# Optimization experiments

Hardware: AMD Instinct MI355X
Metric: run time of the kernel (lower is better)

Reference implementation:

```python
import jax, jax.numpy as jnp
import numpy as np

SQRT_HALF = 0.7071067811865476
DILATIONS = [3 ** (i % 4) for i in range(8)]  # [1,3,9,27,1,3,9,27]


def conv1d(x, w, b, dilation=1):
    # x: [B, Cin, L], w: [Cout, Cin, K], 'same' padding
    out = jax.lax.conv_general_dilated(
        x, w, window_strides=(1,), padding='SAME',
        rhs_dilation=(dilation,),
        dimension_numbers=('NCH', 'OIH', 'NCH'))
    return out + b[None, :, None]


def encoder(x, enc_start_w, enc_start_b, glu_w, glu_b, enc_end_w, enc_end_b):
    # EncoderAny (eval mode -> dropout is identity)
    h = conv1d(x, enc_start_w, enc_start_b)                  # [B, mid, N]
    for i in range(len(DILATIONS)):
        g = conv1d(h, glu_w[i], glu_b[i], dilation=DILATIONS[i])  # [B, 2*mid, N]
        a, b = jnp.split(g, 2, axis=1)
        h = (h + a * jax.nn.sigmoid(b)) * SQRT_HALF           # GLU + residual
    out = conv1d(h, enc_end_w, enc_end_b)                     # [B, 2*d, N]
    K, V = jnp.split(out, 2, axis=1)                          # each [B, d, N]
    return K, V


def reference(in_s, in_t, c_t,
              enc_start_w, enc_start_b, glu_w, glu_b, enc_end_w, enc_end_b,
              wc_pre, w_pre, b_pre, wc_post, w_post, b_post):
    # ---- encoder: source -> K, V ----
    K_s, V_s = encoder(in_s, enc_start_w, enc_start_b, glu_w, glu_b,
                       enc_end_w, enc_end_b)                  # [B, d, N] each
    d = K_s.shape[1]

    # ---- pre-decoder: target + speaker code -> Q ----
    h_t = in_t + jnp.einsum('bc,cd->bd', c_t, wc_pre)[:, :, None]  # [B, D, T]
    Q_t = conv1d(h_t, w_pre, b_pre)                           # [B, d, T]

    # ---- custom attention: softmax over SOURCE axis (dim=1) ----
    scores = jnp.einsum('bdn,bdt->bnt', K_s, Q_t) / jnp.sqrt(
        jnp.asarray(d, dtype=K_s.dtype))                      # [B, N, T]
    A = jax.nn.softmax(scores, axis=1)                        # softmax over N
    R = jnp.einsum('bdn,bnt->bdt', V_s, A)                    # [B, d, T]

    # concat with Q (dropout p=0.9 in training; eval/deterministic -> identity)
    R = jnp.concatenate([R, Q_t], axis=1)                     # [B, 2d, T]

    # ---- post-decoder: attended features + speaker code -> y ----
    h_r = R + jnp.einsum('bc,cd->bd', c_t, wc_post)[:, :, None]
    y = conv1d(h_r, w_post, b_post)                           # [B, D, T]
    return y, A


def setup_inputs() -> dict:
    key = jax.random.key(0)
    ks = jax.random.split(key, 16)
    B, D, N, T = 16, 240, 2048, 2048
    mid, d, C = 512, 512, 8
    L = len(DILATIONS)

    def w(k, shape, fan_in):
        return (jax.random.normal(k, shape, dtype=jnp.float32)
                / jnp.sqrt(jnp.asarray(fan_in, jnp.float32)))

    return {
        'in_s': jax.random.normal(ks[0], (B, D, N), dtype=jnp.float32),
        'in_t': jax.random.normal(ks[1], (B, D, T), dtype=jnp.float32),
        'c_t': jax.random.normal(ks[2], (B, C), dtype=jnp.float32),
        'enc_start_w': w(ks[3], (mid, D, 1), D),
        'enc_start_b': jnp.zeros((mid,), jnp.float32),
        'glu_w': w(ks[4], (L, 2 * mid, mid, 5), mid * 5),
        'glu_b': jnp.zeros((L, 2 * mid), jnp.float32),
        'enc_end_w': w(ks[5], (2 * d, mid, 1), mid),
        'enc_end_b': jnp.zeros((2 * d,), jnp.float32),
        'wc_pre': w(ks[6], (C, D), C),
        'w_pre': w(ks[7], (d, D, 1), D),
        'b_pre': jnp.zeros((d,), jnp.float32),
        'wc_post': w(ks[8], (C, 2 * d), C),
        'w_post': w(ks[9], (D, 2 * d, 1), 2 * d),
        'b_post': jnp.zeros((D,), jnp.float32),
    }
```

## Files before the change

### kernel.cpp

```cpp
#include <hip/hip_runtime.h>
#include <cstdint>
#include <cstddef>

typedef unsigned short u16;
typedef __attribute__((ext_vector_type(8))) short short8;
typedef __attribute__((ext_vector_type(4))) float f32x4;

static constexpr int BB = 16, DIN = 240, NN = 2048, TT = 2048;
static constexpr long long Y_SIZE = (long long)BB * DIN * TT;
static constexpr float SQRT_HALF_F = 0.70710678118654752440f;
static constexpr int HPAD = 64;
static constexpr int HROWS = NN + 2 * HPAD;

#define DEVI __device__ __forceinline__

DEVI u16 f2bf(float f) {
    unsigned u = __builtin_bit_cast(unsigned, f);
    u += 0x7FFFu + ((u >> 16) & 1u);
    return (u16)(u >> 16);
}
DEVI float bf2f(u16 h) {
    unsigned u = ((unsigned)h) << 16;
    return __builtin_bit_cast(float, u);
}

DEVI void gld16(const void* g, const void* l) {
    __builtin_amdgcn_global_load_lds(
        (const __attribute__((address_space(1))) unsigned int*)g,
        (__attribute__((address_space(3))) unsigned int*)l, 16, 0, 0);
}

DEVI int glu_perm(int g) {
    int tile = g >> 8, r = g & 255;
    int wcq = r >> 6, r2 = r & 63;
    int n = r2 >> 4, fr = r2 & 15;
    return tile * 128 + wcq * 32 + (n >> 1) * 16 + fr + (n & 1) * 512;
}

struct GemmP {
    const u16* A; long long a_bstride; int lda;
    const u16* Bw; long long b_bstride; long long b_tapstride; int ldb;
    int ntaps; int shift0; int dshift; int Kt; int ks_log2;
    void* out; long long o_bstride; int ldc;
    const float* bias; int bias_bstride;
    float scale;
    int store_ncols;
};

#define FENCE() asm volatile("" ::: "memory")
#define SBAR()  do { FENCE(); __builtin_amdgcn_s_barrier(); FENCE(); } while (0)

template <int OUTK>
__global__ __launch_bounds__(512, 2)
void gemm256(GemmP p, int tilesM, int tilesN) {
    __shared__ __align__(16) u16 As[2][256 * 64];
    __shared__ __align__(16) u16 Bs[2][256 * 64];
    const int tid = threadIdx.x;
    const int lane = tid & 63;
    const int wv = tid >> 6;
    const int wr = wv >> 2, wcq = wv & 3;
    const int fr = lane & 15, fq = lane >> 4;

    const int nwg = gridDim.x;
    int widx = (blockIdx.x & 7) * (nwg >> 3) + (blockIdx.x >> 3);
    const int mt = widx % tilesM; widx /= tilesM;
    const int nt = widx % tilesN;
    const int bz = widx / tilesN;
    const int n0 = mt * 256, c0 = nt * 256;

    const int lda = p.lda, ldb = p.ldb;
    const u16* Abase = p.A + (long long)bz * p.a_bstride;
    const u16* Bbase = p.Bw + (long long)bz * p.b_bstride;
    const int kmask = (1 << p.ks_log2) - 1;
    const int tot = p.ntaps << p.ks_log2;

    f32x4 acc[8][4];
#pragma unroll
    for (int m = 0; m < 8; ++m)
#pragma unroll
        for (int n = 0; n < 4; ++n) acc[m][n] = (f32x4){0.f, 0.f, 0.f, 0.f};

    const int srow = lane >> 3, sslot = lane & 7;
    const int js = (sslot ^ srow) << 3;
    const int sr0 = wv * 16 + srow;

    const long long sA8 = 8LL * lda, sAh = 128LL * lda;
    const long long sB8 = 8LL * ldb, sBh = 128LL * ldb;
    const long long dAtap = (long long)p.dshift * lda - (long long)kmask * 64;
    const long long dBtap = p.b_tapstride - (long long)kmask * 64;

    auto aAddr = [&](int t) -> const u16* {
        int tap = t >> p.ks_log2;
        return Abase + (long long)(n0 + p.shift0 + tap * p.dshift + sr0) * lda
               + ((t & kmask) << 6) + js;
    };
    auto bAddr = [&](int t) -> const u16* {
        int tap = t >> p.ks_log2;
        return Bbase + (long long)tap * p.b_tapstride
               + (long long)(c0 + sr0) * ldb + ((t & kmask) << 6) + js;
    };

    u16* uA = &As[0][wv * 1024];
    u16* uB = &Bs[0][wv * 1024];

    {
        const u16* a0 = aAddr(0);
        gld16(a0, uA);              gld16(a0 + sA8, uA + 512);
        gld16(a0 + sAh, uA + 8192); gld16(a0 + sAh + sA8, uA + 8192 + 512);
        const u16* b0 = bAddr(0);
        gld16(b0, uB);              gld16(b0 + sB8, uB + 512);
        gld16(b0 + sBh, uB + 8192); gld16(b0 + sBh + sB8, uB + 8192 + 512);
        const u16* b1 = bAddr(1);
        gld16(b1, uB + 16384);              gld16(b1 + sB8, uB + 16384 + 512);
        gld16(b1 + sBh, uB + 16384 + 8192); gld16(b1 + sBh + sB8, uB + 16384 + 8192 + 512);
    }
    const u16* aP = aAddr(1);
    const u16* bP = bAddr(2);
    asm volatile("s_waitcnt vmcnt(4)" ::: "memory");
    __builtin_amdgcn_s_barrier();
    FENCE();

    const int aoff0 = (wr * 128 + fr) * 64 + ((fq ^ (fr & 7)) << 3);
    const int aoff1 = (wr * 128 + fr) * 64 + (((4 + fq) ^ (fr & 7)) << 3);
    const int boff0 = (wcq * 64 + fr) * 64 + ((fq ^ (fr & 7)) << 3);
    const int boff1 = (wcq * 64 + fr) * 64 + (((4 + fq) ^ (fr & 7)) << 3);

    short8 af0[4][2], af1[4][2], bf0[2][2], bf1[2][2];

#define READ_AQ(DEST, MQ)                                                      \
    _Pragma("unroll")                                                          \
    for (int mi = 0; mi < 4; ++mi) {                                           \
        DEST[mi][0] = *(const short8*)&Ab[aoff0 + ((MQ) * 64 + mi * 16) * 64]; \
        DEST[mi][1] = *(const short8*)&Ab[aoff1 + ((MQ) * 64 + mi * 16) * 64]; \
    }
#define READ_BQ(BF, NQ)                                                        \
    _Pragma("unroll")                                                          \
    for (int ni = 0; ni < 2; ++ni) {                                           \
        BF[ni][0] = *(const short8*)&Bb[boff0 + ((NQ) * 32 + ni * 16) * 64];   \
        BF[ni][1] = *(const short8*)&Bb[boff1 + ((NQ) * 32 + ni * 16) * 64];   \
    }
#define MFMA_Q2(MQ, NQ, AF, BF)                                                \
    __builtin_amdgcn_s_setprio(1);                                             \
    _Pragma("unroll")                                                          \
    for (int mi = 0; mi < 4; ++mi) {                                           \
        _Pragma("unroll")                                                      \
        for (int ni = 0; ni < 2; ++ni) {                                       \
            _Pragma("unroll")                                                  \
            for (int kk = 0; kk < 2; ++kk)                                     \
                acc[(MQ) * 4 + mi][(NQ) * 2 + ni] =                            \
                    __builtin_amdgcn_mfma_f32_16x16x32_bf16(                   \
                        AF[mi][kk], BF[ni][kk],                                \
                        acc[(MQ) * 4 + mi][(NQ) * 2 + ni], 0, 0, 0);           \
        }                                                                      \
    }                                                                          \
    __builtin_amdgcn_s_setprio(0)

#define TILEBODY(BUF_, DO_A_, DO_B_, STEPA_, STEPB_, VM_)                      \
  {                                                                            \
    const u16* Ab = &As[BUF_][0];                                              \
    const u16* Bb = &Bs[BUF_][0];                                              \
    \
    READ_AQ(af0, 0);                                                           \
    READ_BQ(bf0, 0);                                                           \
    READ_BQ(bf1, 1);                                                           \
    if (DO_A_) { gld16(aP, uA + ((BUF_) ^ 1) * 16384);                         \
                 gld16(aP + sA8, uA + ((BUF_) ^ 1) * 16384 + 512); }           \
    MFMA_Q2(0, 0, af0, bf0);                                                   \
    if (DO_A_) { gld16(aP + sAh, uA + ((BUF_) ^ 1) * 16384 + 8192);            \
                 gld16(aP + sAh + sA8, uA + ((BUF_) ^ 1) * 16384 + 8192 + 512);\
                 aP += (STEPA_); }                                             \
    MFMA_Q2(0, 1, af0, bf1);                                                   \
    SBAR();                                                                    \
                  \
    READ_AQ(af1, 1);                                                           \
    if (DO_B_) { gld16(bP, uB + (BUF_) * 16384);                               \
                 gld16(bP + sB8, uB + (BUF_) * 16384 + 512); }                 \
    MFMA_Q2(1, 1, af1, bf1);                                                   \
    if (DO_B_) { gld16(bP + sBh, uB + (BUF_) * 16384 + 8192);                  \
                 gld16(bP + sBh + sB8, uB + (BUF_) * 16384 + 8192 + 512);      \
                 bP += (STEPB_); }                                             \
    MFMA_Q2(1, 0, af1, bf0);                                                   \
    if ((VM_) == 4) asm volatile("s_waitcnt vmcnt(4)" ::: "memory");           \
    else if ((VM_) == 0) asm volatile("s_waitcnt vmcnt(0)" ::: "memory");      \
    SBAR();                                                                    \
  }

    int t = 0;
    for (; t + 3 < tot; t += 2) {
        const long long stA1 = (((t + 2) & kmask) != 0) ? 64 : dAtap;
        const long long stA2 = (((t + 3) & kmask) != 0) ? 64 : dAtap;
        const long long stB1 = (((t + 3) & kmask) != 0) ? 64 : dBtap;
        const long long stB2 = (((t + 4) & kmask) != 0) ? 64 : dBtap;
        TILEBODY(0, 1, 1, stA1, stB1, 4);
        TILEBODY(1, 1, 1, stA2, stB2, 4);
    }
    TILEBODY(0, 1, 0, 0, 0, 0);
    TILEBODY(1, 0, 0, 0, 0, -1);
#undef READ_AQ
#undef READ_BQ
#undef MFMA_Q2
#undef TILEBODY

    if constexpr (OUTK == 4) {
        const float* bp = p.bias;
#pragma unroll
        for (int m = 0; m < 8; ++m) {
#pragma unroll
            for (int pr = 0; pr < 2; ++pr) {
                int ca = c0 + wcq * 64 + (2 * pr) * 16 + fr;
                int chan = (c0 >> 1) + wcq * 32 + pr * 16 + fr;
                float biasa = bp[ca], biasb = bp[ca + 16];
#pragma unroll
                for (int r = 0; r < 4; ++r) {
                    int row = n0 + wr * 128 + m * 16 + fq * 4 + r;
                    float a = acc[m][2 * pr][r] + biasa;
                    float bq = acc[m][2 * pr + 1][r] + biasb;
                    float sig = 1.f / (1.f + __expf(-bq));
                    float h = bf2f(Abase[(long long)row * lda + chan]);
                    ((u16*)p.out)[(long long)bz * p.o_bstride + (long long)row * p.ldc + chan]
                        = f2bf((h + a * sig) * SQRT_HALF_F);
                }
            }
        }
        return;
    } else if constexpr (OUTK == 2) {
        const float* bias = p.bias + (long long)bz * p.bias_bstride;
#pragma unroll
        for (int m = 0; m < 8; ++m) {
#pragma unroll
            for (int n = 0; n < 4; ++n) {
                int col = c0 + wcq * 64 + n * 16 + fr;
                if (col >= p.store_ncols) continue;
                float cb = bias[col];
#pragma unroll
                for (int r = 0; r < 4; ++r) {
                    int row = n0 + wr * 128 + m * 16 + fq * 4 + r;
                    ((float*)p.out)[(long long)bz * p.o_bstride + (long long)col * p.ldc + row]
                        = acc[m][n][r] * p.scale + cb;
                }
            }
        }
        return;
    } else {
        const float* bias = p.bias ? p.bias + (long long)bz * p.bias_bstride : nullptr;
#pragma unroll
        for (int m = 0; m < 8; ++m) {
#pragma unroll
            for (int n = 0; n < 4; ++n) {
                int col = c0 + wcq * 64 + n * 16 + fr;
                float cb = (OUTK == 1 && bias) ? bias[col] : 0.f;
#pragma unroll
                for (int r = 0; r < 4; ++r) {
                    int row = n0 + wr * 128 + m * 16 + fq * 4 + r;
                    float v = acc[m][n][r] * p.scale + cb;
                    if (OUTK == 5) v += bias[row];
                    ((u16*)p.out)[(long long)bz * p.o_bstride + (long long)row * p.ldc + col]
                        = f2bf(v);
                }
            }
        }
    }
}


__global__ void cvt_glu(const float* src, u16* dst) {
    long long t = (long long)blockIdx.x * blockDim.x + threadIdx.x;
    const long long total = 8LL * 5 * 1024 * 512;
    if (t >= total) return;
    int i = (int)(t % 512); long long r = t / 512;
    int g = (int)(r % 1024); r /= 1024;
    int k = (int)(r % 5); int l = (int)(r / 5);
    int o = glu_perm(g);
    dst[t] = f2bf(src[(((long long)l * 1024 + o) * 512 + i) * 5 + k]);
}

__global__ void perm_bias(const float* gb, float* biasP) {
    int t = blockIdx.x * 256 + threadIdx.x;
    if (t >= 8 * 1024) return;
    int g = t & 1023, l = t >> 10;
    biasP[t] = gb[l * 1024 + glu_perm(g)];
}

__global__ void cvt_pad(const float* src, u16* dst, int Os, int Is, int Od, int Id) {
    long long t = (long long)blockIdx.x * blockDim.x + threadIdx.x;
    if (t >= (long long)Od * Id) return;
    int i = (int)(t % Id); int o = (int)(t / Id);
    float v = (o < Os && i < Is) ? src[(long long)o * Is + i] : 0.f;
    dst[t] = f2bf(v);
}

__global__ void transpose_in(const float* src, u16* dst, int Csrc, int Cdst, int Len) {
    __shared__ float tile[32][33];
    int b = blockIdx.z;
    int n0 = blockIdx.x * 32, c0 = blockIdx.y * 32;
    int tx = threadIdx.x, ty = threadIdx.y;
    int c = c0 + ty, n = n0 + tx;
    float v = 0.f;
    if (c < Csrc) v = src[((long long)b * Csrc + c) * Len + n];
    tile[ty][tx] = v;
    __syncthreads();
    dst[((long long)b * Len + (n0 + ty)) * Cdst + (c0 + tx)] = f2bf(tile[tx][ty]);
}

__global__ void zero_pads(u16* h) {
    long long t = (long long)blockIdx.x * blockDim.x + threadIdx.x;
    const long long total = (long long)BB * 128 * 512;
    if (t >= total) return;
    int c = (int)(t % 512); long long r = t / 512;
    int rr = (int)(r % 128); int b = (int)(r / 128);
    int row = rr < HPAD ? rr : (HROWS - 128 + rr);
    h[((long long)b * HROWS + row) * 512 + c] = 0;
}

__global__ void prebias_kernel(const float* ct, const float* wcpre, const float* wpre,
                               const float* bpre, float* qbias) {
    __shared__ float s[240];
    int b = blockIdx.x; int tid = threadIdx.x;
    if (tid < 240) {
        float a = 0.f;
        for (int c = 0; c < 8; ++c) a += ct[b * 8 + c] * wcpre[c * 240 + tid];
        s[tid] = a;
    }
    __syncthreads();
    for (int o = tid; o < 512; o += 256) {
        float a = bpre[o];
        for (int d0 = 0; d0 < 240; ++d0) a += wpre[o * 240 + d0] * s[d0];
        qbias[b * 512 + o] = a;
    }
}

__global__ void postbias_kernel(const float* ct, const float* wcpost, const float* wpost,
                                const float* bpost, float* ybias) {
    __shared__ float s[1024];
    int b = blockIdx.x; int tid = threadIdx.x;
    for (int e = tid; e < 1024; e += 256) {
        float a = 0.f;
        for (int c = 0; c < 8; ++c) a += ct[b * 8 + c] * wcpost[c * 1024 + e];
        s[e] = a;
    }
    __syncthreads();
    if (tid < 240) {
        float a = bpost[tid];
        for (int e = 0; e < 1024; ++e) a += wpost[tid * 1024 + e] * s[e];
        ybias[b * 240 + tid] = a;
    }
}

__global__ __launch_bounds__(256)
void softmax_rows(const u16* St, u16* AT) {
    int b = blockIdx.y;
    int t = blockIdx.x * 4 + (threadIdx.x >> 6);
    int lane = threadIdx.x & 63;
    const u16* row = St + ((long long)b * TT + t) * NN;
    short8 v[4];
#pragma unroll
    for (int i = 0; i < 4; ++i) v[i] = ((const short8*)row)[i * 64 + lane];
    float f[32];
#pragma unroll
    for (int i = 0; i < 4; ++i)
#pragma unroll
        for (int j = 0; j < 8; ++j) f[i * 8 + j] = bf2f((u16)v[i][j]);
    float m = -3.4e38f;
#pragma unroll
    for (int i = 0; i < 32; ++i) m = fmaxf(m, f[i]);
#pragma unroll
    for (int s = 1; s < 64; s <<= 1) m = fmaxf(m, __shfl_xor(m, s, 64));
    float sum = 0.f;
#pragma unroll
    for (int i = 0; i < 32; ++i) { f[i] = __expf(f[i] - m); sum += f[i]; }
#pragma unroll
    for (int s = 1; s < 64; s <<= 1) sum += __shfl_xor(sum, s, 64);
    float li = 1.f / sum;
    u16* atrow = AT + ((long long)b * TT + t) * NN;
#pragma unroll
    for (int i = 0; i < 4; ++i) {
        short8 pk;
#pragma unroll
        for (int j = 0; j < 8; ++j) pk[j] = (short)f2bf(f[i * 8 + j] * li);
        ((short8*)atrow)[i * 64 + lane] = pk;
    }
}

__global__ void transpose_out(const u16* AT, float* A) {
    __shared__ float tile[32][33];
    int b = blockIdx.z;
    int n0 = blockIdx.x * 32, t0 = blockIdx.y * 32;
    int tx = threadIdx.x, ty = threadIdx.y;
#pragma unroll
    for (int k = 0; k < 4; ++k) {
        int t = t0 + ty + k * 8;
        tile[ty + k * 8][tx] = bf2f(AT[((long long)b * TT + t) * NN + n0 + tx]);
    }
    __syncthreads();
#pragma unroll
    for (int k = 0; k < 4; ++k) {
        int n = n0 + ty + k * 8;
        A[((long long)b * NN + n) * TT + t0 + tx] = tile[tx][ty + k * 8];
    }
}


extern "C" void kernel_launch(void* const* d_in, const int* in_sizes, int n_in,
                              void* d_out, int out_size, void* d_ws, size_t ws_size,
                              hipStream_t stream) {
    const float* in_s        = (const float*)d_in[0];
    const float* in_t        = (const float*)d_in[1];
    const float* c_t         = (const float*)d_in[2];
    const float* enc_start_w = (const float*)d_in[3];
    const float* enc_start_b = (const float*)d_in[4];
    const float* glu_w       = (const float*)d_in[5];
    const float* glu_b       = (const float*)d_in[6];
    const float* enc_end_w   = (const float*)d_in[7];
    const float* enc_end_b   = (const float*)d_in[8];
    const float* wc_pre      = (const float*)d_in[9];
    const float* w_pre       = (const float*)d_in[10];
    const float* b_pre       = (const float*)d_in[11];
    const float* wc_post     = (const float*)d_in[12];
    const float* w_post      = (const float*)d_in[13];
    const float* b_post      = (const float*)d_in[14];

    char* w = (char*)d_ws;
    u16* wglu   = (u16*)w; w += 8LL * 5 * 1024 * 512 * 2;
    u16* wstart = (u16*)w; w += 512LL * 256 * 2;
    u16* wend   = (u16*)w; w += 1024LL * 512 * 2;
    u16* wpre   = (u16*)w; w += 512LL * 256 * 2;
    u16* wpost  = (u16*)w; w += 256LL * 1024 * 2;
    u16* XS     = (u16*)w; w += (long long)BB * NN * 256 * 2;
    u16* XT     = (u16*)w; w += (long long)BB * TT * 256 * 2;
    u16* h0     = (u16*)w; w += (long long)BB * HROWS * 512 * 2;
    u16* h1     = (u16*)w; w += (long long)BB * HROWS * 512 * 2;
    u16* Kb     = (u16*)w; w += (long long)BB * NN * 512 * 2;
    u16* Vb     = (u16*)w; w += (long long)BB * 512 * NN * 2;
    u16* Rc     = (u16*)w; w += (long long)BB * TT * 1024 * 2;
    u16* ATb    = (u16*)w; w += (long long)BB * TT * NN * 2;
    float* qbias = (float*)w; w += 16LL * 512 * 4;
    float* ybias = (float*)w; w += 16LL * 256 * 4;
    float* biasP = (float*)w; w += 8LL * 1024 * 4;
    if ((size_t)(w - (char*)d_ws) > ws_size) return;

    float* yout = (float*)d_out;
    float* Areg = yout + Y_SIZE;
    u16* Sbf = (u16*)Areg;

    cvt_glu<<<(8LL * 5 * 1024 * 512 + 255) / 256, 256, 0, stream>>>(glu_w, wglu);
    perm_bias<<<(8 * 1024 + 255) / 256, 256, 0, stream>>>(glu_b, biasP);
    cvt_pad<<<(512 * 256 + 255) / 256, 256, 0, stream>>>(enc_start_w, wstart, 512, 240, 512, 256);
    cvt_pad<<<(1024 * 512 + 255) / 256, 256, 0, stream>>>(enc_end_w, wend, 1024, 512, 1024, 512);
    cvt_pad<<<(512 * 256 + 255) / 256, 256, 0, stream>>>(w_pre, wpre, 512, 240, 512, 256);
    cvt_pad<<<(256 * 1024 + 255) / 256, 256, 0, stream>>>(w_post, wpost, 240, 1024, 256, 1024);
    transpose_in<<<dim3(NN / 32, 256 / 32, BB), dim3(32, 32), 0, stream>>>(in_s, XS, 240, 256, NN);
    transpose_in<<<dim3(TT / 32, 256 / 32, BB), dim3(32, 32), 0, stream>>>(in_t, XT, 240, 256, TT);
    zero_pads<<<((long long)BB * 128 * 512 + 255) / 256, 256, 0, stream>>>(h0);
    zero_pads<<<((long long)BB * 128 * 512 + 255) / 256, 256, 0, stream>>>(h1);
    prebias_kernel<<<16, 256, 0, stream>>>(c_t, wc_pre, w_pre, b_pre, qbias);
    postbias_kernel<<<16, 256, 0, stream>>>(c_t, wc_post, w_post, b_post, ybias);

    {
        GemmP p{}; p.A = XS; p.a_bstride = (long long)NN * 256; p.lda = 256;
        p.Bw = wstart; p.b_bstride = 0; p.b_tapstride = 0; p.ldb = 256;
        p.ntaps = 1; p.shift0 = 0; p.dshift = 0; p.Kt = 256; p.ks_log2 = 2;
        p.out = h0 + HPAD * 512; p.o_bstride = (long long)HROWS * 512; p.ldc = 512;
        p.bias = enc_start_b; p.bias_bstride = 0; p.scale = 1.f; p.store_ncols = 512;
        gemm256<1><<<8 * 2 * 16, 512, 0, stream>>>(p, 8, 2);
    }

    const int dils[8] = {1, 3, 9, 27, 1, 3, 9, 27};
    u16* hin = h0; u16* hout = h1;
    for (int l = 0; l < 8; ++l) {
        GemmP q{}; q.A = hin + HPAD * 512; q.a_bstride = (long long)HROWS * 512; q.lda = 512;
        q.Bw = wglu + (long long)l * 5 * 1024 * 512; q.b_bstride = 0;
        q.b_tapstride = 1024LL * 512; q.ldb = 512;
        q.ntaps = 5; q.shift0 = -2 * dils[l]; q.dshift = dils[l]; q.Kt = 512; q.ks_log2 = 3;
        q.out = hout + HPAD * 512; q.o_bstride = (long long)HROWS * 512; q.ldc = 512;
        q.bias = biasP + l * 1024; q.bias_bstride = 0; q.scale = 1.f; q.store_ncols = 1024;
        gemm256<4><<<8 * 4 * 16, 512, 0, stream>>>(q, 8, 4);
        u16* tmp = hin; hin = hout; hout = tmp;
    }

    {
        GemmP p{}; p.A = hin + HPAD * 512; p.a_bstride = (long long)HROWS * 512; p.lda = 512;
        p.Bw = wend; p.b_bstride = 0; p.b_tapstride = 0; p.ldb = 512;
        p.ntaps = 1; p.shift0 = 0; p.dshift = 0; p.Kt = 512; p.ks_log2 = 3;
        p.out = Kb; p.o_bstride = (long long)NN * 512; p.ldc = 512;
        p.bias = enc_end_b; p.bias_bstride = 0; p.scale = 1.f; p.store_ncols = 512;
        gemm256<1><<<8 * 2 * 16, 512, 0, stream>>>(p, 8, 2);
    }
    {
        GemmP p{}; p.A = wend + 512LL * 512; p.a_bstride = 0; p.lda = 512;
        p.Bw = hin + HPAD * 512; p.b_bstride = (long long)HROWS * 512; p.b_tapstride = 0; p.ldb = 512;
        p.ntaps = 1; p.shift0 = 0; p.dshift = 0; p.Kt = 512; p.ks_log2 = 3;
        p.out = Vb; p.o_bstride = 512LL * NN; p.ldc = NN;
        p.bias = enc_end_b + 512; p.bias_bstride = 0; p.scale = 1.f; p.store_ncols = NN;
        gemm256<5><<<2 * 8 * 16, 512, 0, stream>>>(p, 2, 8);
    }

    {
        GemmP p{}; p.A = XT; p.a_bstride = (long long)TT * 256; p.lda = 256;
        p.Bw = wpre; p.b_bstride = 0; p.b_tapstride = 0; p.ldb = 256;
        p.ntaps = 1; p.shift0 = 0; p.dshift = 0; p.Kt = 256; p.ks_log2 = 2;
        p.out = Rc + 512; p.o_bstride = (long long)TT * 1024; p.ldc = 1024;
        p.bias = qbias; p.bias_bstride = 512; p.scale = 1.f; p.store_ncols = 512;
        gemm256<1><<<8 * 2 * 16, 512, 0, stream>>>(p, 8, 2);
    }

    {
        GemmP p{}; p.A = Rc + 512; p.a_bstride = (long long)TT * 1024; p.lda = 1024;
        p.Bw = Kb; p.b_bstride = (long long)NN * 512; p.b_tapstride = 0; p.ldb = 512;
        p.ntaps = 1; p.shift0 = 0; p.dshift = 0; p.Kt = 512; p.ks_log2 = 3;
        p.out = Sbf; p.o_bstride = (long long)TT * NN; p.ldc = NN;
        p.bias = nullptr; p.bias_bstride = 0; p.scale = 0.04419417382415922f;
        p.store_ncols = NN;
        gemm256<1><<<8 * 8 * 16, 512, 0, stream>>>(p, 8, 8);
    }

    softmax_rows<<<dim3(TT / 4, BB), 256, 0, stream>>>(Sbf, ATb);
    transpose_out<<<dim3(NN / 32, TT / 32, BB), dim3(32, 8), 0, stream>>>(ATb, Areg);

    {
        GemmP p{}; p.A = ATb; p.a_bstride = (long long)TT * NN; p.lda = NN;
        p.Bw = Vb; p.b_bstride = 512LL * NN; p.b_tapstride = 0; p.ldb = NN;
        p.ntaps = 1; p.shift0 = 0; p.dshift = 0; p.Kt = NN; p.ks_log2 = 5;
        p.out = Rc; p.o_bstride = (long long)TT * 1024; p.ldc = 1024;
        p.bias = nullptr; p.bias_bstride = 0; p.scale = 1.f; p.store_ncols = 512;
        gemm256<1><<<8 * 2 * 16, 512, 0, stream>>>(p, 8, 2);
    }

    {
        GemmP p{}; p.A = Rc; p.a_bstride = (long long)TT * 1024; p.lda = 1024;
        p.Bw = wpost; p.b_bstride = 0; p.b_tapstride = 0; p.ldb = 1024;
        p.ntaps = 1; p.shift0 = 0; p.dshift = 0; p.Kt = 1024; p.ks_log2 = 4;
        p.out = yout; p.o_bstride = (long long)DIN * TT; p.ldc = TT;
        p.bias = ybias; p.bias_bstride = 240; p.scale = 1.f; p.store_ncols = 240;
        gemm256<2><<<8 * 1 * 16, 512, 0, stream>>>(p, 8, 1);
    }
}
```

Baseline: 1.749 ms.

## Triple-buffer B tiles in LDS and drop the mid-tile barrier

Expands the B-operand LDS staging from two buffers to three and rotates read/write pointers each iteration. The B prefetch for a future tile then never targets the buffer being read, so the barrier in the middle of each tile body is removed. The second A-fragment LDS read is also hoisted earlier to overlap with MFMAs. This cuts synchronization stalls per K-step. In exchange, LDS use rises to 160KB per block, the whole LDS of a CU, which keeps it at one block per CU and adds pointer-rotation bookkeeping.

```diff
diff --git a/kernel.cpp b/kernel.cpp
--- a/kernel.cpp
+++ b/kernel.cpp
@@ -54,7 +54,7 @@
 __global__ __launch_bounds__(512, 2)
 void gemm256(GemmP p, int tilesM, int tilesN) {
     __shared__ __align__(16) u16 As[2][256 * 64];
-    __shared__ __align__(16) u16 Bs[2][256 * 64];
+    __shared__ __align__(16) u16 Bs[3][256 * 64];
     const int tid = threadIdx.x;
     const int lane = tid & 63;
     const int wv = tid >> 6;
@@ -83,6 +83,7 @@
     const int srow = lane >> 3, sslot = lane & 7;
     const int js = (sslot ^ srow) << 3;
     const int sr0 = wv * 16 + srow;
+    const int wvB = wv * 1024;
 
     const long long sA8 = 8LL * lda, sAh = 128LL * lda;
     const long long sB8 = 8LL * ldb, sBh = 128LL * ldb;
@@ -100,19 +101,24 @@
                + (long long)(c0 + sr0) * ldb + ((t & kmask) << 6) + js;
     };
 
-    u16* uA = &As[0][wv * 1024];
-    u16* uB = &Bs[0][wv * 1024];
+    u16* uA = &As[0][wvB];
+
+    u16* pB0 = &Bs[0][0];
+    u16* pB1 = &Bs[1][0];
+    u16* pB2 = &Bs[2][0];
 
     {
         const u16* a0 = aAddr(0);
         gld16(a0, uA);              gld16(a0 + sA8, uA + 512);
         gld16(a0 + sAh, uA + 8192); gld16(a0 + sAh + sA8, uA + 8192 + 512);
         const u16* b0 = bAddr(0);
-        gld16(b0, uB);              gld16(b0 + sB8, uB + 512);
-        gld16(b0 + sBh, uB + 8192); gld16(b0 + sBh + sB8, uB + 8192 + 512);
+        u16* d0 = pB0 + wvB;
+        gld16(b0, d0);              gld16(b0 + sB8, d0 + 512);
+        gld16(b0 + sBh, d0 + 8192); gld16(b0 + sBh + sB8, d0 + 8192 + 512);
         const u16* b1 = bAddr(1);
-        gld16(b1, uB + 16384);              gld16(b1 + sB8, uB + 16384 + 512);
-        gld16(b1 + sBh, uB + 16384 + 8192); gld16(b1 + sBh + sB8, uB + 16384 + 8192 + 512);
+        u16* d1 = pB1 + wvB;
+        gld16(b1, d1);              gld16(b1 + sB8, d1 + 512);
+        gld16(b1 + sBh, d1 + 8192); gld16(b1 + sBh + sB8, d1 + 8192 + 512);
     }
     const u16* aP = aAddr(1);
     const u16* bP = bAddr(2);
@@ -155,29 +161,27 @@
     }                                                                          \
     __builtin_amdgcn_s_setprio(0)
 
-#define TILEBODY(BUF_, DO_A_, DO_B_, STEPA_, STEPB_, VM_)                      \
+#define TILEBODY(BUF_, BRD_, BST_, DO_A_, DO_B_, STEPA_, STEPB_, VM_)          \
   {                                                                            \
     const u16* Ab = &As[BUF_][0];                                              \
-    const u16* Bb = &Bs[BUF_][0];                                              \
-    \
+    const u16* Bb = (BRD_);                                                    \
+    u16* bDst = (BST_) + wvB;                                                  \
     READ_AQ(af0, 0);                                                           \
     READ_BQ(bf0, 0);                                                           \
     READ_BQ(bf1, 1);                                                           \
     if (DO_A_) { gld16(aP, uA + ((BUF_) ^ 1) * 16384);                         \
                  gld16(aP + sA8, uA + ((BUF_) ^ 1) * 16384 + 512); }           \
     MFMA_Q2(0, 0, af0, bf0);                                                   \
+    READ_AQ(af1, 1);                                                           \
     if (DO_A_) { gld16(aP + sAh, uA + ((BUF_) ^ 1) * 16384 + 8192);            \
                  gld16(aP + sAh + sA8, uA + ((BUF_) ^ 1) * 16384 + 8192 + 512);\
                  aP += (STEPA_); }                                             \
     MFMA_Q2(0, 1, af0, bf1);                                                   \
-    SBAR();                                                                    \
-                  \
-    READ_AQ(af1, 1);                                                           \
-    if (DO_B_) { gld16(bP, uB + (BUF_) * 16384);                               \
-                 gld16(bP + sB8, uB + (BUF_) * 16384 + 512); }                 \
+    if (DO_B_) { gld16(bP, bDst);                                              \
+                 gld16(bP + sB8, bDst + 512); }                                \
     MFMA_Q2(1, 1, af1, bf1);                                                   \
-    if (DO_B_) { gld16(bP + sBh, uB + (BUF_) * 16384 + 8192);                  \
-                 gld16(bP + sBh + sB8, uB + (BUF_) * 16384 + 8192 + 512);      \
+    if (DO_B_) { gld16(bP + sBh, bDst + 8192);                                 \
+                 gld16(bP + sBh + sB8, bDst + 8192 + 512);                     \
                  bP += (STEPB_); }                                             \
     MFMA_Q2(1, 0, af1, bf0);                                                   \
     if ((VM_) == 4) asm volatile("s_waitcnt vmcnt(4)" ::: "memory");           \
@@ -191,11 +195,12 @@
         const long long stA2 = (((t + 3) & kmask) != 0) ? 64 : dAtap;
         const long long stB1 = (((t + 3) & kmask) != 0) ? 64 : dBtap;
         const long long stB2 = (((t + 4) & kmask) != 0) ? 64 : dBtap;
-        TILEBODY(0, 1, 1, stA1, stB1, 4);
-        TILEBODY(1, 1, 1, stA2, stB2, 4);
-    }
-    TILEBODY(0, 1, 0, 0, 0, 0);
-    TILEBODY(1, 0, 0, 0, 0, -1);
+        TILEBODY(0, pB0, pB2, 1, 1, stA1, stB1, 4);
+        TILEBODY(1, pB1, pB0, 1, 1, stA2, stB2, 4);
+        u16* tmpB = pB0; pB0 = pB2; pB2 = pB1; pB1 = tmpB;
+    }
+    TILEBODY(0, pB0, pB2, 1, 0, 0, 0, 0);
+    TILEBODY(1, pB1, pB0, 0, 0, 0, 0, -1);
 #undef READ_AQ
 #undef READ_BQ
 #undef MFMA_Q2
```

Measured after the change: 1.678 ms. 4.0% less time.
